# Optimization experiments

Hardware: AMD Instinct MI355X
Metric: run time of the kernel (lower is better)

The kernel has to match this reference:

```python
import jax, jax.numpy as jnp
import numpy as np

WINDOW = 8
NUM_HEADS = 12


def setup_inputs() -> dict:
    key = jax.random.key(0)
    k1, k2, k3 = jax.random.split(key, 3)
    B, H, W, C = 32, 64, 64, 384
    x = jax.random.normal(k1, (B, H, W, C), dtype=jnp.float32)
    w_qkv = jax.random.normal(k2, (C, 3 * C), dtype=jnp.float32) * (C ** -0.5)
    w_proj = jax.random.normal(k3, (C, C), dtype=jnp.float32) * (C ** -0.5)
    b_proj = jnp.zeros((C,), dtype=jnp.float32)
    return {"x": x, "w_qkv": w_qkv, "w_proj": w_proj, "b_proj": b_proj}


def window_partition(x, ws):
    B, H, W, C = x.shape
    x = x.reshape(B, H // ws, ws, W // ws, ws, C)
    x = x.transpose(0, 1, 3, 2, 4, 5)  # [B, nH, nW, ws, ws, C]
    return x.reshape(-1, ws * ws, C)


def window_reverse(x, ws, H, W):
    nWin = (H // ws) * (W // ws)
    B = x.shape[0] // nWin
    C = x.shape[2]
    x = x.reshape(B, H // ws, W // ws, ws, ws, C)
    x = x.transpose(0, 1, 3, 2, 4, 5)
    return x.reshape(B, H, W, C)


def reference(x, w_qkv, w_proj, b_proj):
    B, H, W, C = x.shape
    ws = WINDOW
    nh = NUM_HEADS
    hd = C // nh
    scale = hd ** -0.5
    N = ws * ws

    xw = window_partition(x, ws)                      # [nW*B, N, C]
    qkv = xw @ w_qkv                                  # [nW*B, N, 3C]
    qkv = qkv.reshape(-1, N, 3, nh, hd)
    qkv = qkv.transpose(2, 0, 3, 1, 4)                # [3, nW*B, nh, N, hd]
    q, k, v = qkv[0], qkv[1], qkv[2]

    attn = jnp.einsum('whnd,whmd->whnm', q, k) * scale  # [nW*B, nh, N, N]
    attn = jax.nn.softmax(attn, axis=-1)
    out = jnp.einsum('whnm,whmd->whnd', attn, v)         # [nW*B, nh, N, hd]
    out = out.transpose(0, 2, 1, 3).reshape(-1, N, C)    # [nW*B, N, C]
    out = out @ w_proj + b_proj
    return window_reverse(out, ws, H, W)
```

## Files before the change

### kernel.cpp

```cpp
#include <hip/hip_runtime.h>


typedef __attribute__((ext_vector_type(8))) short bf16x8;
typedef __attribute__((ext_vector_type(4))) float f32x4;
typedef __attribute__((ext_vector_type(4))) short short4_t;

__device__ __forceinline__ short f2bf(float f) {
    union { float f; unsigned u; } v; v.f = f;
    unsigned r = v.u + 0x7fffu + ((v.u >> 16) & 1u);
    return (short)(r >> 16);
}

__device__ __forceinline__ unsigned pk2(float a, float b) {
    return ((unsigned)(unsigned short)f2bf(b) << 16) | (unsigned short)f2bf(a);
}

__device__ __forceinline__ f32x4 mfma16(bf16x8 a, bf16x8 b, f32x4 c) {
    return __builtin_amdgcn_mfma_f32_16x16x32_bf16(a, b, c, 0, 0, 0);
}

__device__ __forceinline__ short4_t pack4(f32x4 v) {
    short4_t s;
    s.x = f2bf(v[0]); s.y = f2bf(v[1]); s.z = f2bf(v[2]); s.w = f2bf(v[3]);
    return s;
}

__device__ __forceinline__ void gload_lds16(const void* g, void* l) {
    __builtin_amdgcn_global_load_lds(
        (const __attribute__((address_space(1))) unsigned int*)g,
        (__attribute__((address_space(3))) unsigned int*)l, 16, 0, 0);
}

__device__ __forceinline__ void drain_vmem() {
    asm volatile("s_waitcnt vmcnt(0)" ::: "memory");
    __builtin_amdgcn_sched_barrier(0);
}

__global__ void prep_weights(const float* __restrict__ wqkv, const float* __restrict__ wproj,
                             short* __restrict__ wq_sw, short* __restrict__ wp_t) {
    const int QKV_ELEMS = 12 * 96 * 384;
    int i = blockIdx.x * 256 + threadIdx.x;
    if (i < QKV_ELEMS) {
        int h = i / (96 * 384);
        int o = i % (96 * 384);
        int row = o / 384;
        int kb = ((o % 384) * 2) ^ ((row & 7) << 4);
        int k = kb >> 1;
        int col = (row >> 5) * 384 + h * 32 + (row & 31);
        float w = wqkv[k * 1152 + col];
        if (row < 32) w *= 0.17677669529663687f;
        wq_sw[i] = f2bf(w);
    } else if (i < QKV_ELEMS + 384 * 384) {
        int j = i - QKV_ELEMS;
        int n = j / 384, k = j % 384;
        wp_t[j] = f2bf(wproj[k * 384 + n]);
    }
}

__global__ __launch_bounds__(512, 4)
void qkv_attn(const float* __restrict__ x, const short* __restrict__ wq_sw,
              short* __restrict__ y_sw) {
    __shared__ short Wl[48 * 384];
    __shared__ short k_s[2][64 * 40];
    __shared__ short v_t[2][32 * 72];
    __shared__ short ps[2][64 * 72];

    const int tid   = threadIdx.x;
    const int lane  = tid & 63;
    const int wid   = tid >> 6;
    const int col16 = lane & 15;
    const int kgrp  = lane >> 4;
    const int w     = wid >> 2;
    const int quad  = wid & 3;

    const int win = blockIdx.x * 2 + w;
    const int b = win >> 6, wi = win & 63, whr = wi >> 3, wwc = wi & 7;
    const float* xbase = x + (((b * 64) + whr * 8) * 64 + wwc * 8) * 384;

    for (int i = wid; i < 36; i += 8)
        gload_lds16(wq_sw + i * 512 + lane * 8, &Wl[i * 512]);

    bf16x8 xf[12];
    {
        int t = quad * 16 + col16;
        const float* xr = xbase + ((t >> 3) * 64 + (t & 7)) * 384;
#pragma unroll
        for (int kk = 0; kk < 12; ++kk) {
            const float* p0 = xr + kk * 32 + kgrp * 8;
            float4 a = *reinterpret_cast<const float4*>(p0);
            float4 c = *reinterpret_cast<const float4*>(p0 + 4);
            bf16x8 f;
            f[0] = f2bf(a.x); f[1] = f2bf(a.y); f[2] = f2bf(a.z); f[3] = f2bf(a.w);
            f[4] = f2bf(c.x); f[5] = f2bf(c.y); f[6] = f2bf(c.z); f[7] = f2bf(c.w);
            xf[kk] = f;
        }
    }

    const int g = win * 64 + quad * 16 + col16;
    const int mtile = g >> 7, yrow = g & 127;
    char* ybase = (char*)y_sw + (size_t)mtile * 98304 + (size_t)yrow * 128;

    for (int h = 0; h < 12; ++h) {
        drain_vmem();
        __syncthreads();

        f32x4 aQ0 = (f32x4){0.f, 0.f, 0.f, 0.f};
        f32x4 aQ1 = (f32x4){0.f, 0.f, 0.f, 0.f};
        f32x4 aK0 = (f32x4){0.f, 0.f, 0.f, 0.f};
#pragma unroll
        for (int kk = 0; kk < 12; ++kk) {
            const int kbyte = (kk * 32 + kgrp * 8) * 2;
            const int r0 = col16, r1 = 16 + col16, r2 = 32 + col16;
            bf16x8 wf0 = *reinterpret_cast<const bf16x8*>(
                (const char*)Wl + r0 * 768 + (kbyte ^ ((r0 & 7) << 4)));
            bf16x8 wf1 = *reinterpret_cast<const bf16x8*>(
                (const char*)Wl + r1 * 768 + (kbyte ^ ((r1 & 7) << 4)));
            bf16x8 wf2 = *reinterpret_cast<const bf16x8*>(
                (const char*)Wl + r2 * 768 + (kbyte ^ ((r2 & 7) << 4)));
            aQ0 = mfma16(wf0, xf[kk], aQ0);
            aQ1 = mfma16(wf1, xf[kk], aQ1);
            aK0 = mfma16(wf2, xf[kk], aK0);
        }

        __syncthreads();

        {
            const short* src = wq_sw + h * (96 * 384) + 48 * 384;
            for (int i = wid; i < 36; i += 8)
                gload_lds16(src + i * 512 + lane * 8, &Wl[i * 512]);
        }

        bf16x8 qa;
        {
            unsigned A0 = pk2(aQ0[0], aQ0[1]);
            unsigned A1 = pk2(aQ0[2], aQ0[3]);
            unsigned B0 = pk2(aQ1[0], aQ1[1]);
            unsigned B1 = pk2(aQ1[2], aQ1[3]);
            int s0 = ((kgrp & 1) * 2) * 16 + col16;
            int a0 = __shfl((int)A0, s0, 64),      a1 = __shfl((int)A1, s0, 64);
            int a2 = __shfl((int)A0, s0 + 16, 64), a3 = __shfl((int)A1, s0 + 16, 64);
            int b0 = __shfl((int)B0, s0, 64),      b1 = __shfl((int)B1, s0, 64);
            int b2 = __shfl((int)B0, s0 + 16, 64), b3 = __shfl((int)B1, s0 + 16, 64);
            union { int i[4]; bf16x8 v; } qu;
            const bool loHalf = (kgrp < 2);
            qu.i[0] = loHalf ? a0 : b0;
            qu.i[1] = loHalf ? a1 : b1;
            qu.i[2] = loHalf ? a2 : b2;
            qu.i[3] = loHalf ? a3 : b3;
            qa = qu.v;
        }
        *reinterpret_cast<short4_t*>(
            &k_s[w][(quad * 16 + col16) * 40 + kgrp * 4]) = pack4(aK0);

        drain_vmem();
        __syncthreads();

        f32x4 aK1 = (f32x4){0.f, 0.f, 0.f, 0.f};
        f32x4 aV0 = (f32x4){0.f, 0.f, 0.f, 0.f};
        f32x4 aV1 = (f32x4){0.f, 0.f, 0.f, 0.f};
#pragma unroll
        for (int kk = 0; kk < 12; ++kk) {
            const int kbyte = (kk * 32 + kgrp * 8) * 2;
            const int r0 = col16, r1 = 16 + col16, r2 = 32 + col16;
            bf16x8 wfK = *reinterpret_cast<const bf16x8*>(
                (const char*)Wl + r0 * 768 + (kbyte ^ ((r0 & 7) << 4)));
            bf16x8 wfV0 = *reinterpret_cast<const bf16x8*>(
                (const char*)Wl + r1 * 768 + (kbyte ^ ((r1 & 7) << 4)));
            bf16x8 wfV1 = *reinterpret_cast<const bf16x8*>(
                (const char*)Wl + r2 * 768 + (kbyte ^ ((r2 & 7) << 4)));
            aK1 = mfma16(wfK, xf[kk], aK1);
            aV0 = mfma16(xf[kk], wfV0, aV0);
            aV1 = mfma16(xf[kk], wfV1, aV1);
        }
        *reinterpret_cast<short4_t*>(
            &k_s[w][(quad * 16 + col16) * 40 + 16 + kgrp * 4]) = pack4(aK1);
        *reinterpret_cast<short4_t*>(
            &v_t[w][(col16) * 72 + quad * 16 + kgrp * 4]) = pack4(aV0);
        *reinterpret_cast<short4_t*>(
            &v_t[w][(16 + col16) * 72 + quad * 16 + kgrp * 4]) = pack4(aV1);

        __syncthreads();

        if (h < 11) {
            const short* src = wq_sw + (h + 1) * (96 * 384);
            for (int i = wid; i < 36; i += 8)
                gload_lds16(src + i * 512 + lane * 8, &Wl[i * 512]);
        }

        f32x4 sc[4];
#pragma unroll
        for (int nt = 0; nt < 4; ++nt) {
            bf16x8 kf = *reinterpret_cast<const bf16x8*>(
                &k_s[w][(nt * 16 + col16) * 40 + kgrp * 8]);
            f32x4 z = (f32x4){0.f, 0.f, 0.f, 0.f};
            sc[nt] = mfma16(qa, kf, z);
        }
        float mx[4], sm[4];
#pragma unroll
        for (int r = 0; r < 4; ++r)
            mx[r] = fmaxf(fmaxf(sc[0][r], sc[1][r]), fmaxf(sc[2][r], sc[3][r]));
#pragma unroll
        for (int d = 1; d < 16; d <<= 1)
#pragma unroll
            for (int r = 0; r < 4; ++r) mx[r] = fmaxf(mx[r], __shfl_xor(mx[r], d, 16));
#pragma unroll
        for (int r = 0; r < 4; ++r) {
            sm[r] = 0.f;
#pragma unroll
            for (int nt = 0; nt < 4; ++nt) {
                sc[nt][r] = __expf(sc[nt][r] - mx[r]); sm[r] += sc[nt][r];
            }
        }
#pragma unroll
        for (int d = 1; d < 16; d <<= 1)
#pragma unroll
            for (int r = 0; r < 4; ++r) sm[r] += __shfl_xor(sm[r], d, 16);
#pragma unroll
        for (int r = 0; r < 4; ++r) {
            float inv = 1.0f / sm[r];
            int prow = quad * 16 + kgrp * 4 + r;
#pragma unroll
            for (int nt = 0; nt < 4; ++nt)
                ps[w][prow * 72 + nt * 16 + col16] = f2bf(sc[nt][r] * inv);
        }
        f32x4 o2[2];
        o2[0] = (f32x4){0.f, 0.f, 0.f, 0.f};
        o2[1] = (f32x4){0.f, 0.f, 0.f, 0.f};
#pragma unroll
        for (int kt = 0; kt < 2; ++kt) {
            bf16x8 pb = *reinterpret_cast<const bf16x8*>(
                &ps[w][(quad * 16 + col16) * 72 + kt * 32 + kgrp * 8]);
#pragma unroll
            for (int d = 0; d < 2; ++d) {
                bf16x8 va = *reinterpret_cast<const bf16x8*>(
                    &v_t[w][(d * 16 + col16) * 72 + kt * 32 + kgrp * 8]);
                o2[d] = mfma16(va, pb, o2[d]);
            }
        }
#pragma unroll
        for (int d = 0; d < 2; ++d) {
            int c0 = h * 32 + d * 16 + kgrp * 4;
            int kchunk = c0 >> 6;
            int koff = (2 * (c0 & 63)) ^ ((yrow & 7) << 4);
            *reinterpret_cast<short4_t*>(ybase + kchunk * 16384 + koff) = pack4(o2[d]);
        }
    }
}

__global__ __launch_bounds__(256)
void proj_gemm(const short* __restrict__ y_sw, const short* __restrict__ wp_t,
               const float* __restrict__ b_proj, float* __restrict__ out) {
    __shared__ short At[2][128 * 64];

    const int tid = threadIdx.x, lane = tid & 63, wv = tid >> 6;
    const int col16 = lane & 15, kgrp = lane >> 4;
    const int wm = wv >> 1, wn = wv & 1;
    const int mtile = blockIdx.x;
    const int nblk  = blockIdx.y;

    const short* asrc = y_sw + (size_t)mtile * 6 * 128 * 64;

    for (int i = wv; i < 16; i += 4)
        gload_lds16(asrc + i * 512 + lane * 8, &At[0][i * 512]);

    const short* bptr[4];
#pragma unroll
    for (int nt = 0; nt < 4; ++nt)
        bptr[nt] = wp_t + (size_t)(nblk * 128 + wn * 64 + nt * 16 + col16) * 384;

    f32x4 acc[4][4];
#pragma unroll
    for (int i = 0; i < 4; ++i)
#pragma unroll
        for (int j = 0; j < 4; ++j) acc[i][j] = (f32x4){0.f, 0.f, 0.f, 0.f};

    int cur = 0;
    for (int ks = 0; ks < 6; ++ks) {
        drain_vmem();
        __syncthreads();
        if (ks < 5) {
            const short* src = asrc + (ks + 1) * (128 * 64);
            for (int i = wv; i < 16; i += 4)
                gload_lds16(src + i * 512 + lane * 8, &At[cur ^ 1][i * 512]);
        }
#pragma unroll
        for (int kk = 0; kk < 2; ++kk) {
            const int kbyte = kk * 64 + kgrp * 16;
            bf16x8 af[4];
#pragma unroll
            for (int mt = 0; mt < 4; ++mt) {
                const int r = wm * 64 + mt * 16 + col16;
                af[mt] = *reinterpret_cast<const bf16x8*>(
                    (const char*)At[cur] + r * 128 + (kbyte ^ ((r & 7) << 4)));
            }
#pragma unroll
            for (int nt = 0; nt < 4; ++nt) {
                bf16x8 bf = *reinterpret_cast<const bf16x8*>(bptr[nt] + ks * 64 + kk * 32 + kgrp * 8);
#pragma unroll
                for (int mt = 0; mt < 4; ++mt)
                    acc[mt][nt] = mfma16(af[mt], bf, acc[mt][nt]);
            }
        }
        cur ^= 1;
    }

#pragma unroll
    for (int nt = 0; nt < 4; ++nt) {
        int c = nblk * 128 + wn * 64 + nt * 16 + col16;
        float bias = b_proj[c];
#pragma unroll
        for (int mt = 0; mt < 4; ++mt) {
#pragma unroll
            for (int r = 0; r < 4; ++r) {
                int gg = mtile * 128 + wm * 64 + mt * 16 + kgrp * 4 + r;
                int win = gg >> 6, t = gg & 63;
                int b = win >> 6, whr = (win >> 3) & 7, wwc = win & 7;
                int orow = (b * 64 + whr * 8 + (t >> 3)) * 64 + wwc * 8 + (t & 7);
                out[(size_t)orow * 384 + c] = acc[mt][nt][r] + bias;
            }
        }
    }
}

__global__ __launch_bounds__(512, 2)
void win_attn_fused(const float* __restrict__ x, const short* __restrict__ wq_sw,
                    const short* __restrict__ wp_t, const float* __restrict__ b_proj,
                    float* __restrict__ out) {
    __shared__ short Wl[96 * 384];
    __shared__ short q_s[2][64 * 40];
    __shared__ short k_s[2][64 * 40];
    __shared__ short v_t[2][32 * 72];
    __shared__ short ps[2][64 * 72];

    const int tid   = threadIdx.x;
    const int lane  = tid & 63;
    const int wv    = tid >> 6;
    const int col16 = lane & 15;
    const int kgrp  = lane >> 4;
    const int wwin  = wv >> 2;
    const int q4    = wv & 3;
    const int wm    = q4 >> 1, wn = q4 & 1;

    const int win = blockIdx.x * 2 + wwin;
    const int b = win >> 6, wi = win & 63, whr = wi >> 3, wwc = wi & 7;
    const float* xbase = x + (((b * 64) + whr * 8) * 64 + wwc * 8) * 384;

    for (int i = 0; i < 9; ++i) {
        int chunk = wv * 9 + i;
        gload_lds16(wq_sw + chunk * 512 + lane * 8, &Wl[chunk * 512]);
    }
    bf16x8 xf[12];
    {
        int t = q4 * 16 + col16;
        const float* xr = xbase + ((t >> 3) * 64 + (t & 7)) * 384;
#pragma unroll
        for (int kk = 0; kk < 12; ++kk) {
            const float* p0 = xr + kk * 32 + kgrp * 8;
            float4 a = *reinterpret_cast<const float4*>(p0);
            float4 c = *reinterpret_cast<const float4*>(p0 + 4);
            bf16x8 f;
            f[0] = f2bf(a.x); f[1] = f2bf(a.y); f[2] = f2bf(a.z); f[3] = f2bf(a.w);
            f[4] = f2bf(c.x); f[5] = f2bf(c.y); f[6] = f2bf(c.z); f[7] = f2bf(c.w);
            xf[kk] = f;
        }
    }
    f32x4 pacc[2][12];
#pragma unroll
    for (int i = 0; i < 2; ++i)
#pragma unroll
        for (int j = 0; j < 12; ++j) pacc[i][j] = (f32x4){0.f, 0.f, 0.f, 0.f};

    for (int h = 0; h < 12; ++h) {
        drain_vmem();
        __syncthreads();
        f32x4 acc[6];
#pragma unroll
        for (int i = 0; i < 6; ++i) acc[i] = (f32x4){0.f, 0.f, 0.f, 0.f};
#pragma unroll
        for (int kk = 0; kk < 12; ++kk) {
            const int kbyte = (kk * 32 + kgrp * 8) * 2;
#pragma unroll
            for (int rd = 0; rd < 6; ++rd) {
                const int row = (rd >> 1) * 32 + (rd & 1) * 16 + col16;
                const bf16x8 wf = *reinterpret_cast<const bf16x8*>(
                    (const char*)Wl + row * 768 + (kbyte ^ ((row & 7) << 4)));
                if (rd < 4) acc[rd] = mfma16(wf, xf[kk], acc[rd]);
                else        acc[rd] = mfma16(xf[kk], wf, acc[rd]);
            }
        }
#pragma unroll
        for (int rd = 0; rd < 4; ++rd) {
            short* dst = (rd < 2) ? q_s[wwin] : k_s[wwin];
            *reinterpret_cast<short4_t*>(
                &dst[(q4 * 16 + col16) * 40 + (rd & 1) * 16 + kgrp * 4]) = pack4(acc[rd]);
        }
#pragma unroll
        for (int d = 0; d < 2; ++d)
            *reinterpret_cast<short4_t*>(
                &v_t[wwin][(d * 16 + col16) * 72 + q4 * 16 + kgrp * 4]) = pack4(acc[4 + d]);

        __syncthreads();
        if (h < 11) {
            const short* src = wq_sw + (h + 1) * (96 * 384);
            for (int i = 0; i < 9; ++i) {
                int chunk = wv * 9 + i;
                gload_lds16(src + chunk * 512 + lane * 8, &Wl[chunk * 512]);
            }
        }
        bf16x8 qa = *reinterpret_cast<const bf16x8*>(
            &q_s[wwin][(q4 * 16 + col16) * 40 + kgrp * 8]);
        f32x4 sc[4];
#pragma unroll
        for (int nt = 0; nt < 4; ++nt) {
            bf16x8 kf = *reinterpret_cast<const bf16x8*>(
                &k_s[wwin][(nt * 16 + col16) * 40 + kgrp * 8]);
            f32x4 z = (f32x4){0.f, 0.f, 0.f, 0.f};
            sc[nt] = mfma16(qa, kf, z);
        }
        float mx[4], sm[4], p[4][4];
#pragma unroll
        for (int r = 0; r < 4; ++r)
            mx[r] = fmaxf(fmaxf(sc[0][r], sc[1][r]), fmaxf(sc[2][r], sc[3][r]));
#pragma unroll
        for (int d = 1; d < 16; d <<= 1)
#pragma unroll
            for (int r = 0; r < 4; ++r) mx[r] = fmaxf(mx[r], __shfl_xor(mx[r], d, 16));
#pragma unroll
        for (int r = 0; r < 4; ++r) {
            sm[r] = 0.f;
#pragma unroll
            for (int nt = 0; nt < 4; ++nt) { p[nt][r] = __expf(sc[nt][r] - mx[r]); sm[r] += p[nt][r]; }
        }
#pragma unroll
        for (int d = 1; d < 16; d <<= 1)
#pragma unroll
            for (int r = 0; r < 4; ++r) sm[r] += __shfl_xor(sm[r], d, 16);
#pragma unroll
        for (int r = 0; r < 4; ++r) {
            float inv = 1.0f / sm[r];
            int prow = q4 * 16 + kgrp * 4 + r;
#pragma unroll
            for (int nt = 0; nt < 4; ++nt)
                ps[wwin][prow * 72 + nt * 16 + col16] = f2bf(p[nt][r] * inv);
        }
        f32x4 o2[2];
        o2[0] = (f32x4){0.f, 0.f, 0.f, 0.f};
        o2[1] = (f32x4){0.f, 0.f, 0.f, 0.f};
#pragma unroll
        for (int kt = 0; kt < 2; ++kt) {
            bf16x8 pb = *reinterpret_cast<const bf16x8*>(
                &ps[wwin][(q4 * 16 + col16) * 72 + kt * 32 + kgrp * 8]);
#pragma unroll
            for (int d = 0; d < 2; ++d) {
                bf16x8 va = *reinterpret_cast<const bf16x8*>(
                    &v_t[wwin][(d * 16 + col16) * 72 + kt * 32 + kgrp * 8]);
                o2[d] = mfma16(va, pb, o2[d]);
            }
        }
#pragma unroll
        for (int d = 0; d < 2; ++d)
            *reinterpret_cast<short4_t*>(
                &ps[wwin][(q4 * 16 + col16) * 72 + d * 16 + kgrp * 4]) = pack4(o2[d]);
        __syncthreads();
#pragma unroll
        for (int mt = 0; mt < 2; ++mt) {
            bf16x8 ya = *reinterpret_cast<const bf16x8*>(
                &ps[wwin][(wm * 32 + mt * 16 + col16) * 72 + kgrp * 8]);
#pragma unroll
            for (int nt = 0; nt < 12; ++nt) {
                bf16x8 wb = *reinterpret_cast<const bf16x8*>(
                    &wp_t[(wn * 192 + nt * 16 + col16) * 384 + h * 32 + kgrp * 8]);
                pacc[mt][nt] = mfma16(ya, wb, pacc[mt][nt]);
            }
        }
    }
#pragma unroll
    for (int nt = 0; nt < 12; ++nt) {
        int c = wn * 192 + nt * 16 + col16;
        float bias = b_proj[c];
#pragma unroll
        for (int mt = 0; mt < 2; ++mt) {
#pragma unroll
            for (int r = 0; r < 4; ++r) {
                int token = wm * 32 + mt * 16 + kgrp * 4 + r;
                int hh = whr * 8 + (token >> 3);
                int ww2 = wwc * 8 + (token & 7);
                out[(((b * 64) + hh) * 64 + ww2) * 384 + c] = pacc[mt][nt][r] + bias;
            }
        }
    }
}

extern "C" void kernel_launch(void* const* d_in, const int* in_sizes, int n_in,
                              void* d_out, int out_size, void* d_ws, size_t ws_size,
                              hipStream_t stream) {
    const float* x     = (const float*)d_in[0];
    const float* wqkv  = (const float*)d_in[1];
    const float* wproj = (const float*)d_in[2];
    const float* bproj = (const float*)d_in[3];

    short* wq_sw = (short*)d_ws;
    short* wp_t  = wq_sw + 12 * 96 * 384;
    short* y_sw  = wp_t + 384 * 384;
    const size_t need = (size_t)(12 * 96 * 384 + 384 * 384) * 2 + (size_t)1024 * 6 * 128 * 128;

    prep_weights<<<2304, 256, 0, stream>>>(wqkv, wproj, wq_sw, wp_t);
    if (ws_size >= need) {
        qkv_attn<<<1024, 512, 0, stream>>>(x, wq_sw, y_sw);
        proj_gemm<<<dim3(1024, 3), 256, 0, stream>>>(y_sw, wp_t, bproj, (float*)d_out);
    } else {
        win_attn_fused<<<1024, 512, 0, stream>>>(x, wq_sw, wp_t, bproj, (float*)d_out);
    }
}
```

Baseline: 379.8 us.

## Store QKV weights in fragment-major order and transpose score MFMA for lane-local softmax

Weight prep now writes the per-head QKV weights in an MFMA fragment-major order, so each lane reads its bf16x8 fragment from LDS at a fixed base plus a constant offset. This replaces the XOR-swizzled address math and is meant to keep reads conflict-free while cutting per-load integer work. The score MFMA now takes its operands swapped, so each lane holds one query row's scores across its registers. The max and sum reductions then need only two cross-lane shuffles instead of four-step shuffles per row. Probabilities are written to LDS as packed 4-element stores instead of scalar stores.

Measured after the change: 317.6 us, median of 2. -16.4%, faster.

```diff
diff --git a/kernel.cpp b/kernel.cpp
--- a/kernel.cpp
+++ b/kernel.cpp
@@ -37,19 +37,23 @@
 }
 
 __global__ void prep_weights(const float* __restrict__ wqkv, const float* __restrict__ wproj,
-                             short* __restrict__ wq_sw, short* __restrict__ wp_t) {
+                             short* __restrict__ wq_fm, short* __restrict__ wp_t) {
     const int QKV_ELEMS = 12 * 96 * 384;
     int i = blockIdx.x * 256 + threadIdx.x;
     if (i < QKV_ELEMS) {
-        int h = i / (96 * 384);
-        int o = i % (96 * 384);
-        int row = o / 384;
-        int kb = ((o % 384) * 2) ^ ((row & 7) << 4);
-        int k = kb >> 1;
-        int col = (row >> 5) * 384 + h * 32 + (row & 31);
+        int e    = i & 7;
+        int f    = i >> 3;
+        int row  = f % 48;
+        int kk   = (f / 48) % 12;
+        int g    = (f / (48 * 12)) % 4;
+        int half = (f / (48 * 12 * 4)) & 1;
+        int h    = f / (48 * 12 * 4 * 2);
+        int grow = half * 48 + row;
+        int k    = kk * 32 + g * 8 + e;
+        int col  = (grow >> 5) * 384 + h * 32 + (grow & 31);
         float w = wqkv[k * 1152 + col];
-        if (row < 32) w *= 0.17677669529663687f;
-        wq_sw[i] = f2bf(w);
+        if (grow < 32) w *= 0.17677669529663687f;
+        wq_fm[i] = f2bf(w);
     } else if (i < QKV_ELEMS + 384 * 384) {
         int j = i - QKV_ELEMS;
         int n = j / 384, k = j % 384;
@@ -58,7 +62,7 @@
 }
 
 __global__ __launch_bounds__(512, 4)
-void qkv_attn(const float* __restrict__ x, const short* __restrict__ wq_sw,
+void qkv_attn(const float* __restrict__ x, const short* __restrict__ wq_fm,
               short* __restrict__ y_sw) {
     __shared__ short Wl[48 * 384];
     __shared__ short k_s[2][64 * 40];
@@ -77,8 +81,10 @@
     const int b = win >> 6, wi = win & 63, whr = wi >> 3, wwc = wi & 7;
     const float* xbase = x + (((b * 64) + whr * 8) * 64 + wwc * 8) * 384;
 
+    const char* Wb = (const char*)Wl + kgrp * 9216 + col16 * 16;
+
     for (int i = wid; i < 36; i += 8)
-        gload_lds16(wq_sw + i * 512 + lane * 8, &Wl[i * 512]);
+        gload_lds16(wq_fm + i * 512 + lane * 8, &Wl[i * 512]);
 
     bf16x8 xf[12];
     {
@@ -109,14 +115,9 @@
         f32x4 aK0 = (f32x4){0.f, 0.f, 0.f, 0.f};
 #pragma unroll
         for (int kk = 0; kk < 12; ++kk) {
-            const int kbyte = (kk * 32 + kgrp * 8) * 2;
-            const int r0 = col16, r1 = 16 + col16, r2 = 32 + col16;
-            bf16x8 wf0 = *reinterpret_cast<const bf16x8*>(
-                (const char*)Wl + r0 * 768 + (kbyte ^ ((r0 & 7) << 4)));
-            bf16x8 wf1 = *reinterpret_cast<const bf16x8*>(
-                (const char*)Wl + r1 * 768 + (kbyte ^ ((r1 & 7) << 4)));
-            bf16x8 wf2 = *reinterpret_cast<const bf16x8*>(
-                (const char*)Wl + r2 * 768 + (kbyte ^ ((r2 & 7) << 4)));
+            bf16x8 wf0 = *reinterpret_cast<const bf16x8*>(Wb + kk * 768);
+            bf16x8 wf1 = *reinterpret_cast<const bf16x8*>(Wb + kk * 768 + 256);
+            bf16x8 wf2 = *reinterpret_cast<const bf16x8*>(Wb + kk * 768 + 512);
             aQ0 = mfma16(wf0, xf[kk], aQ0);
             aQ1 = mfma16(wf1, xf[kk], aQ1);
             aK0 = mfma16(wf2, xf[kk], aK0);
@@ -125,7 +126,7 @@
         __syncthreads();
 
         {
-            const short* src = wq_sw + h * (96 * 384) + 48 * 384;
+            const short* src = wq_fm + h * 36864 + 18432;
             for (int i = wid; i < 36; i += 8)
                 gload_lds16(src + i * 512 + lane * 8, &Wl[i * 512]);
         }
@@ -160,14 +161,9 @@
         f32x4 aV1 = (f32x4){0.f, 0.f, 0.f, 0.f};
 #pragma unroll
         for (int kk = 0; kk < 12; ++kk) {
-            const int kbyte = (kk * 32 + kgrp * 8) * 2;
-            const int r0 = col16, r1 = 16 + col16, r2 = 32 + col16;
-            bf16x8 wfK = *reinterpret_cast<const bf16x8*>(
-                (const char*)Wl + r0 * 768 + (kbyte ^ ((r0 & 7) << 4)));
-            bf16x8 wfV0 = *reinterpret_cast<const bf16x8*>(
-                (const char*)Wl + r1 * 768 + (kbyte ^ ((r1 & 7) << 4)));
-            bf16x8 wfV1 = *reinterpret_cast<const bf16x8*>(
-                (const char*)Wl + r2 * 768 + (kbyte ^ ((r2 & 7) << 4)));
+            bf16x8 wfK  = *reinterpret_cast<const bf16x8*>(Wb + kk * 768);
+            bf16x8 wfV0 = *reinterpret_cast<const bf16x8*>(Wb + kk * 768 + 256);
+            bf16x8 wfV1 = *reinterpret_cast<const bf16x8*>(Wb + kk * 768 + 512);
             aK1 = mfma16(wfK, xf[kk], aK1);
             aV0 = mfma16(xf[kk], wfV0, aV0);
             aV1 = mfma16(xf[kk], wfV1, aV1);
@@ -182,7 +178,7 @@
         __syncthreads();
 
         if (h < 11) {
-            const short* src = wq_sw + (h + 1) * (96 * 384);
+            const short* src = wq_fm + (h + 1) * 36864;
             for (int i = wid; i < 36; i += 8)
                 gload_lds16(src + i * 512 + lane * 8, &Wl[i * 512]);
         }
@@ -193,35 +189,33 @@
             bf16x8 kf = *reinterpret_cast<const bf16x8*>(
                 &k_s[w][(nt * 16 + col16) * 40 + kgrp * 8]);
             f32x4 z = (f32x4){0.f, 0.f, 0.f, 0.f};
-            sc[nt] = mfma16(qa, kf, z);
-        }
-        float mx[4], sm[4];
-#pragma unroll
-        for (int r = 0; r < 4; ++r)
-            mx[r] = fmaxf(fmaxf(sc[0][r], sc[1][r]), fmaxf(sc[2][r], sc[3][r]));
-#pragma unroll
-        for (int d = 1; d < 16; d <<= 1)
-#pragma unroll
-            for (int r = 0; r < 4; ++r) mx[r] = fmaxf(mx[r], __shfl_xor(mx[r], d, 16));
-#pragma unroll
-        for (int r = 0; r < 4; ++r) {
-            sm[r] = 0.f;
-#pragma unroll
-            for (int nt = 0; nt < 4; ++nt) {
-                sc[nt][r] = __expf(sc[nt][r] - mx[r]); sm[r] += sc[nt][r];
-            }
-        }
-#pragma unroll
-        for (int d = 1; d < 16; d <<= 1)
-#pragma unroll
-            for (int r = 0; r < 4; ++r) sm[r] += __shfl_xor(sm[r], d, 16);
-#pragma unroll
-        for (int r = 0; r < 4; ++r) {
-            float inv = 1.0f / sm[r];
-            int prow = quad * 16 + kgrp * 4 + r;
-#pragma unroll
-            for (int nt = 0; nt < 4; ++nt)
-                ps[w][prow * 72 + nt * 16 + col16] = f2bf(sc[nt][r] * inv);
+            sc[nt] = mfma16(kf, qa, z);
+        }
+        float m = sc[0][0];
+#pragma unroll
+        for (int nt = 0; nt < 4; ++nt)
+#pragma unroll
+            for (int r = 0; r < 4; ++r) m = fmaxf(m, sc[nt][r]);
+        m = fmaxf(m, __shfl_xor(m, 16, 64));
+        m = fmaxf(m, __shfl_xor(m, 32, 64));
+        float s = 0.f;
+#pragma unroll
+        for (int nt = 0; nt < 4; ++nt)
+#pragma unroll
+            for (int r = 0; r < 4; ++r) {
+                sc[nt][r] = __expf(sc[nt][r] - m);
+                s += sc[nt][r];
+            }
+        s += __shfl_xor(s, 16, 64);
+        s += __shfl_xor(s, 32, 64);
+        float inv = 1.0f / s;
+#pragma unroll
+        for (int nt = 0; nt < 4; ++nt) {
+            f32x4 pv;
+            pv[0] = sc[nt][0] * inv; pv[1] = sc[nt][1] * inv;
+            pv[2] = sc[nt][2] * inv; pv[3] = sc[nt][3] * inv;
+            *reinterpret_cast<short4_t*>(
+                &ps[w][(quad * 16 + col16) * 72 + nt * 16 + kgrp * 4]) = pack4(pv);
         }
         f32x4 o2[2];
         o2[0] = (f32x4){0.f, 0.f, 0.f, 0.f};
@@ -323,7 +317,7 @@
 }
 
 __global__ __launch_bounds__(512, 2)
-void win_attn_fused(const float* __restrict__ x, const short* __restrict__ wq_sw,
+void win_attn_fused(const float* __restrict__ x, const short* __restrict__ wq_fm,
                     const short* __restrict__ wp_t, const float* __restrict__ b_proj,
                     float* __restrict__ out) {
     __shared__ short Wl[96 * 384];
@@ -345,9 +339,11 @@
     const int b = win >> 6, wi = win & 63, whr = wi >> 3, wwc = wi & 7;
     const float* xbase = x + (((b * 64) + whr * 8) * 64 + wwc * 8) * 384;
 
+    const char* Wb = (const char*)Wl + kgrp * 9216 + col16 * 16;
+
     for (int i = 0; i < 9; ++i) {
         int chunk = wv * 9 + i;
-        gload_lds16(wq_sw + chunk * 512 + lane * 8, &Wl[chunk * 512]);
+        gload_lds16(wq_fm + chunk * 512 + lane * 8, &Wl[chunk * 512]);
     }
     bf16x8 xf[12];
     {
@@ -378,12 +374,10 @@
         for (int i = 0; i < 6; ++i) acc[i] = (f32x4){0.f, 0.f, 0.f, 0.f};
 #pragma unroll
         for (int kk = 0; kk < 12; ++kk) {
-            const int kbyte = (kk * 32 + kgrp * 8) * 2;
 #pragma unroll
             for (int rd = 0; rd < 6; ++rd) {
-                const int row = (rd >> 1) * 32 + (rd & 1) * 16 + col16;
                 const bf16x8 wf = *reinterpret_cast<const bf16x8*>(
-                    (const char*)Wl + row * 768 + (kbyte ^ ((row & 7) << 4)));
+                    Wb + (rd / 3) * 36864 + kk * 768 + (rd % 3) * 256);
                 if (rd < 4) acc[rd] = mfma16(wf, xf[kk], acc[rd]);
                 else        acc[rd] = mfma16(xf[kk], wf, acc[rd]);
             }
@@ -401,7 +395,7 @@
 
         __syncthreads();
         if (h < 11) {
-            const short* src = wq_sw + (h + 1) * (96 * 384);
+            const short* src = wq_fm + (h + 1) * 36864;
             for (int i = 0; i < 9; ++i) {
                 int chunk = wv * 9 + i;
                 gload_lds16(src + chunk * 512 + lane * 8, &Wl[chunk * 512]);
@@ -499,16 +493,16 @@
     const float* wproj = (const float*)d_in[2];
     const float* bproj = (const float*)d_in[3];
 
-    short* wq_sw = (short*)d_ws;
-    short* wp_t  = wq_sw + 12 * 96 * 384;
+    short* wq_fm = (short*)d_ws;
+    short* wp_t  = wq_fm + 12 * 96 * 384;
     short* y_sw  = wp_t + 384 * 384;
     const size_t need = (size_t)(12 * 96 * 384 + 384 * 384) * 2 + (size_t)1024 * 6 * 128 * 128;
 
-    prep_weights<<<2304, 256, 0, stream>>>(wqkv, wproj, wq_sw, wp_t);
+    prep_weights<<<2304, 256, 0, stream>>>(wqkv, wproj, wq_fm, wp_t);
     if (ws_size >= need) {
-        qkv_attn<<<1024, 512, 0, stream>>>(x, wq_sw, y_sw);
+        qkv_attn<<<1024, 512, 0, stream>>>(x, wq_fm, y_sw);
         proj_gemm<<<dim3(1024, 3), 256, 0, stream>>>(y_sw, wp_t, bproj, (float*)d_out);
     } else {
-        win_attn_fused<<<1024, 512, 0, stream>>>(x, wq_sw, wp_t, bproj, (float*)d_out);
-    }
-}
+        win_attn_fused<<<1024, 512, 0, stream>>>(x, wq_fm, wp_t, bproj, (float*)d_out);
+    }
+}
```
